# Kernel tuning notes

Measured on AMD Instinct MI355X. Metric: run time of the kernel, lower is better.

## Reference

```python
import jax, jax.numpy as jnp
import numpy as np

B, T, F, H, OUT, L = 4096, 336, 12, 50, 1, 3


def _lstm_layer(x_tbf, W_ih, W_hh, b_ih, b_hh):
    """PyTorch-semantics LSTM layer. x_tbf: [T,B,in]; returns [T,B,H]."""
    Hh = W_hh.shape[1]
    Bsz = x_tbf.shape[1]
    # precompute input projection for all timesteps: [T,B,4H]
    xz = jnp.einsum('tbf,gf->tbg', x_tbf, W_ih) + (b_ih + b_hh)

    def step(carry, xz_t):
        h, c = carry
        z = xz_t + h @ W_hh.T  # [B,4H]
        i, f, g, o = jnp.split(z, 4, axis=-1)  # PyTorch gate order i,f,g,o
        c = jax.nn.sigmoid(f) * c + jax.nn.sigmoid(i) * jnp.tanh(g)
        h = jax.nn.sigmoid(o) * jnp.tanh(c)
        return (h, c), h

    h0 = jnp.zeros((Bsz, Hh), x_tbf.dtype)
    c0 = jnp.zeros((Bsz, Hh), x_tbf.dtype)
    _, hs = jax.lax.scan(step, (h0, c0), xz)
    return hs


def setup_inputs() -> dict:
    key = jax.random.key(0)
    ks = jax.random.split(key, 16)
    s = 1.0 / np.sqrt(H)  # PyTorch LSTM init scale
    inp = {"x": jax.random.normal(ks[0], (B, T, F), dtype=jnp.float32)}
    in_sizes = [F, H, H]
    k = 1
    for l in range(L):
        inp[f"W_ih_{l}"] = jax.random.uniform(ks[k], (4 * H, in_sizes[l]), jnp.float32, -s, s); k += 1
        inp[f"W_hh_{l}"] = jax.random.uniform(ks[k], (4 * H, H), jnp.float32, -s, s); k += 1
        inp[f"b_ih_{l}"] = jax.random.uniform(ks[k], (4 * H,), jnp.float32, -s, s); k += 1
        inp[f"b_hh_{l}"] = jax.random.uniform(ks[k], (4 * H,), jnp.float32, -s, s); k += 1
    inp["W_lin"] = jax.random.uniform(ks[13], (OUT, H), jnp.float32, -s, s)
    inp["b_lin"] = jax.random.uniform(ks[14], (OUT,), jnp.float32, -s, s)
    return inp


def reference(x, W_ih_0, W_hh_0, b_ih_0, b_hh_0,
              W_ih_1, W_hh_1, b_ih_1, b_hh_1,
              W_ih_2, W_hh_2, b_ih_2, b_hh_2,
              W_lin, b_lin):
    h = jnp.transpose(x, (1, 0, 2))  # [T,B,F] time-major for scan
    params = [(W_ih_0, W_hh_0, b_ih_0, b_hh_0),
              (W_ih_1, W_hh_1, b_ih_1, b_hh_1),
              (W_ih_2, W_hh_2, b_ih_2, b_hh_2)]
    for W_ih, W_hh, bi, bh in params:
        h = _lstm_layer(h, W_ih, W_hh, bi, bh)  # [T,B,H]
    last = h[-1]  # out[:, -1, :] in batch_first layout
    return last @ W_lin.T + b_lin  # [B,OUT]
```

## Files before the change

kernel.cpp:

```cpp
#include <hip/hip_runtime.h>


#define Bsz 4096
#define Tt  336
#define BT  16
#define NTH 1024

typedef _Float16 half8 __attribute__((ext_vector_type(8)));
typedef float    floatx4 __attribute__((ext_vector_type(4)));

struct __align__(16) SMem {
  _Float16 act0[2][BT * 64];
  _Float16 act1[2][BT * 128];
  _Float16 act2[2][BT * 128];
};

__device__ __forceinline__ int offA0(int n, int L) {
  return n * 64 + ((((L >> 3) ^ n) & 7) << 3) + (L & 7);
}
__device__ __forceinline__ int offA12(int n, int L) {
  return n * 128 + ((((L >> 3) ^ n) & 15) << 3) + (L & 7);
}

__device__ __forceinline__ float lstm_cell(floatx4 z, float& c) {
  float ei = __builtin_amdgcn_exp2f(z[0]);
  float ef = __builtin_amdgcn_exp2f(z[1]);
  float eg = __builtin_amdgcn_exp2f(z[2]);
  float eo = __builtin_amdgcn_exp2f(z[3]);
  float ig = __builtin_amdgcn_rcpf(1.f + ei);
  float fg = __builtin_amdgcn_rcpf(1.f + ef);
  float rg = __builtin_amdgcn_rcpf(1.f + eg);
  float og = __builtin_amdgcn_rcpf(1.f + eo);
  float gg = 1.f - 2.f * rg;
  c = fg * c + ig * gg;
  float ec = __builtin_amdgcn_exp2f(2.885390082f * c);
  float rc = __builtin_amdgcn_rcpf(1.f + ec);
  return og * (1.f - 2.f * rc);
}

__device__ __forceinline__ half8 wfrag(const float* __restrict__ Wih,
                                       const float* __restrict__ Whh,
                                       int lenih, int bound, int R, int k0) {
  half8 r = {};
  int u = R >> 2, g = R & 3;
  float sc = (g == 2) ? 2.885390082f : -1.442695041f;
  if (u < 50) {
    int row = g * 50 + u;
#pragma unroll
    for (int j = 0; j < 8; ++j) {
      int k = k0 + j;
      float v = 0.f;
      if (k < bound)           v = Wih[row * lenih + k];
      else if (k < bound + 50) v = Whh[row * 50 + (k - bound)];
      r[j] = (_Float16)(sc * v);
    }
  }
  return r;
}

#define MFMA(a, b, acc) __builtin_amdgcn_mfma_f32_16x16x32_f16((a), (b), (acc), 0, 0, 0)

__global__ __launch_bounds__(NTH, 4)
void lstm_mfma_kernel(const float* __restrict__ x,
                      const float* __restrict__ Wih0, const float* __restrict__ Whh0,
                      const float* __restrict__ bih0, const float* __restrict__ bhh0,
                      const float* __restrict__ Wih1, const float* __restrict__ Whh1,
                      const float* __restrict__ bih1, const float* __restrict__ bhh1,
                      const float* __restrict__ Wih2, const float* __restrict__ Whh2,
                      const float* __restrict__ bih2, const float* __restrict__ bhh2,
                      const float* __restrict__ Wlin, const float* __restrict__ blin,
                      float* __restrict__ out) {
  __shared__ SMem sm;
  const int tid  = threadIdx.x;
  const int blk  = blockIdx.x;
  const int lane = tid & 63;
  const int w    = tid >> 6;
  const int n    = lane & 15;
  const int q    = lane >> 4;

  {
    int* zp = (int*)&sm;
    for (int i = tid; i < (int)(sizeof(SMem) / 4); i += NTH) zp[i] = 0;
  }

  int Lw, nc, mm3[3] = {0, 0, 0};
  switch (w) {
    case 0:  Lw = 0; nc = 3; mm3[0] = 0;  mm3[1] = 1;  mm3[2] = 2;  break;
    case 1:  Lw = 0; nc = 2; mm3[0] = 3;  mm3[1] = 4;               break;
    case 2:  Lw = 0; nc = 3; mm3[0] = 5;  mm3[1] = 6;  mm3[2] = 7;  break;
    case 3:  Lw = 0; nc = 2; mm3[0] = 8;  mm3[1] = 9;               break;
    case 4:  Lw = 1; nc = 2; mm3[0] = 0;  mm3[1] = 1;               break;
    case 5:  Lw = 1; nc = 3; mm3[0] = 2;  mm3[1] = 3;  mm3[2] = 4;  break;
    case 6:  Lw = 1; nc = 2; mm3[0] = 5;  mm3[1] = 6;               break;
    case 7:  Lw = 1; nc = 3; mm3[0] = 7;  mm3[1] = 8;  mm3[2] = 9;  break;
    case 8:  Lw = 2; nc = 3; mm3[0] = 0;  mm3[1] = 1;  mm3[2] = 2;  break;
    case 9:  Lw = 2; nc = 2; mm3[0] = 3;  mm3[1] = 4;               break;
    case 10: Lw = 2; nc = 2; mm3[0] = 5;  mm3[1] = 6;               break;
    case 11: Lw = 2; nc = 2; mm3[0] = 7;  mm3[1] = 8;               break;
    case 12: Lw = 2; nc = 2; mm3[0] = 9;  mm3[1] = 10;              break;
    case 13: Lw = 0; nc = 3; mm3[0] = 10; mm3[1] = 11; mm3[2] = 12; break;
    case 14: Lw = 1; nc = 3; mm3[0] = 10; mm3[1] = 11; mm3[2] = 12; break;
    default: Lw = 2; nc = 2; mm3[0] = 11; mm3[1] = 12;              break;
  }
  const float* Wih = (Lw == 0) ? Wih0 : ((Lw == 1) ? Wih1 : Wih2);
  const float* Whh = (Lw == 0) ? Whh0 : ((Lw == 1) ? Whh1 : Whh2);
  const float* bih = (Lw == 0) ? bih0 : ((Lw == 1) ? bih1 : bih2);
  const float* bhh = (Lw == 0) ? bhh0 : ((Lw == 1) ? bhh1 : bhh2);
  const int lenih = (Lw == 0) ? 12 : 50;
  const int nkc   = (Lw == 0) ? 2 : 4;

  half8  af[3][4];
  floatx4 bia[3];
  float  cst[3] = {0.f, 0.f, 0.f};
  int    woA[3], woB[3];
  bool   uokk[3];
#pragma unroll
  for (int i = 0; i < 3; ++i) {
    bia[i] = (floatx4){0, 0, 0, 0};
#pragma unroll
    for (int kc = 0; kc < 4; ++kc) af[i][kc] = (half8){};
    int m = mm3[i];
    int u = 4 * m + q;
    int uc = (u < 50) ? u : 49;
    uokk[i] = (i < nc) && (u < 50);
    if (Lw == 0) { woA[i] = offA0 (n, 12 + uc); woB[i] = offA12(n, uc); }
    else         { woA[i] = offA12(n, 50 + uc); woB[i] = offA12(n, uc); }
    if (i < nc) {
      int R = 16 * m + n;
#pragma unroll
      for (int kc = 0; kc < 4; ++kc)
        if (kc < nkc)
          af[i][kc] = wfrag(Wih, Whh, lenih, lenih, R, kc * 32 + q * 8);
      if (u < 50) {
#pragma unroll
        for (int g = 0; g < 4; ++g) {
          float sc = (g == 2) ? 2.885390082f : -1.442695041f;
          bia[i][g] = sc * (bih[g * 50 + u] + bhh[g * 50 + u]);
        }
      }
    }
  }

  const int ro0[2] = { offA0(n, q * 8), offA0(n, 32 + q * 8) };
  const int ro1[4] = { offA12(n, q * 8),      offA12(n, 32 + q * 8),
                       offA12(n, 64 + q * 8), offA12(n, 96 + q * 8) };

  const int sr = (tid < 192) ? tid / 12 : 0;
  const int sf = (tid < 192) ? tid - sr * 12 : 0;
  const int sxo = offA0(sr, sf);
  const float* xp = x + ((size_t)(blk * BT + sr) * Tt) * 12 + sf;
  float xnext = 0.f;

  __syncthreads();
  if (tid < 192) {
    sm.act0[0][sxo] = (_Float16)xp[0];
    xnext = xp[12];
  }
  __syncthreads();

#define TICK(p, TAU, CHK)                                                  \
  {                                                                        \
    if (Lw == 0) {                                                         \
      if (!(CHK) || (TAU) <= 335) {                                        \
        half8 b0 = *(const half8*)&sm.act0[p][ro0[0]];                     \
        half8 b1 = *(const half8*)&sm.act0[p][ro0[1]];                     \
        for (int i = 0; i < 3; ++i) if (i < nc) {                          \
          floatx4 z = bia[i];                                              \
          z = MFMA(af[i][0], b0, z);                                       \
          z = MFMA(af[i][1], b1, z);                                       \
          float h = lstm_cell(z, cst[i]);                                  \
          _Float16 hh = (_Float16)h;                                       \
          if (uokk[i]) { sm.act0[1 - (p)][woA[i]] = hh;                    \
                         sm.act1[1 - (p)][woB[i]] = hh; }                  \
        }                                                                  \
      }                                                                    \
    } else if (Lw == 1) {                                                  \
      if (!(CHK) || ((TAU) >= 1 && (TAU) <= 336)) {                        \
        half8 b0 = *(const half8*)&sm.act1[p][ro1[0]];                     \
        half8 b1 = *(const half8*)&sm.act1[p][ro1[1]];                     \
        half8 b2 = *(const half8*)&sm.act1[p][ro1[2]];                     \
        half8 b3 = *(const half8*)&sm.act1[p][ro1[3]];                     \
        for (int i = 0; i < 3; ++i) if (i < nc) {                          \
          floatx4 z = bia[i];                                              \
          z = MFMA(af[i][0], b0, z);                                       \
          z = MFMA(af[i][1], b1, z);                                       \
          z = MFMA(af[i][2], b2, z);                                       \
          z = MFMA(af[i][3], b3, z);                                       \
          float h = lstm_cell(z, cst[i]);                                  \
          _Float16 hh = (_Float16)h;                                       \
          if (uokk[i]) { sm.act1[1 - (p)][woA[i]] = hh;                    \
                         sm.act2[1 - (p)][woB[i]] = hh; }                  \
        }                                                                  \
      }                                                                    \
    } else {                                                               \
      if (!(CHK) || ((TAU) >= 2)) {                                        \
        half8 b0 = *(const half8*)&sm.act2[p][ro1[0]];                     \
        half8 b1 = *(const half8*)&sm.act2[p][ro1[1]];                     \
        half8 b2 = *(const half8*)&sm.act2[p][ro1[2]];                     \
        half8 b3 = *(const half8*)&sm.act2[p][ro1[3]];                     \
        for (int i = 0; i < 3; ++i) if (i < nc) {                          \
          floatx4 z = bia[i];                                              \
          z = MFMA(af[i][0], b0, z);                                       \
          z = MFMA(af[i][1], b1, z);                                       \
          z = MFMA(af[i][2], b2, z);                                       \
          z = MFMA(af[i][3], b3, z);                                       \
          float h = lstm_cell(z, cst[i]);                                  \
          if (uokk[i]) sm.act2[1 - (p)][woA[i]] = (_Float16)h;             \
        }                                                                  \
      }                                                                    \
    }                                                                      \
    if (tid < 192) {                                                       \
      if ((TAU) + 1 < Tt) sm.act0[1 - (p)][sxo] = (_Float16)xnext;         \
      xnext = ((TAU) + 2 < Tt) ? xp[((TAU) + 2) * 12] : 0.f;               \
    }                                                                      \
    __syncthreads();                                                       \
  }

  TICK(0, 0, 1)
  TICK(1, 1, 1)
#pragma unroll 1
  for (int t = 2; t < Tt; t += 2) {
    TICK(0, t, 0)
    TICK(1, t + 1, 0)
  }
  TICK(0, 336, 1)
  TICK(1, 337, 1)
#undef TICK

  if (tid < BT) {
    float s = blin[0];
    for (int uu = 0; uu < 50; ++uu)
      s += Wlin[uu] * (float)sm.act2[0][offA12(tid, 50 + uu)];
    out[blk * BT + tid] = s;
  }
}

extern "C" void kernel_launch(void* const* d_in, const int* in_sizes, int n_in,
                              void* d_out, int out_size, void* d_ws, size_t ws_size,
                              hipStream_t stream) {
  const float* x    = (const float*)d_in[0];
  const float* Wih0 = (const float*)d_in[1];
  const float* Whh0 = (const float*)d_in[2];
  const float* bih0 = (const float*)d_in[3];
  const float* bhh0 = (const float*)d_in[4];
  const float* Wih1 = (const float*)d_in[5];
  const float* Whh1 = (const float*)d_in[6];
  const float* bih1 = (const float*)d_in[7];
  const float* bhh1 = (const float*)d_in[8];
  const float* Wih2 = (const float*)d_in[9];
  const float* Whh2 = (const float*)d_in[10];
  const float* bih2 = (const float*)d_in[11];
  const float* bhh2 = (const float*)d_in[12];
  const float* Wlin = (const float*)d_in[13];
  const float* blin = (const float*)d_in[14];
  float* outp = (float*)d_out;

  dim3 grid(Bsz / BT);
  dim3 block(NTH);
  lstm_mfma_kernel<<<grid, block, 0, stream>>>(
      x, Wih0, Whh0, bih0, bhh0, Wih1, Whh1, bih1, bhh1,
      Wih2, Whh2, bih2, bhh2, Wlin, blin, outp);
}
```

Before: 405.3 us.

## Prefetch input-projection operands one tick ahead to deepen the layer wavefront

```diff
diff --git a/kernel.cpp b/kernel.cpp
--- a/kernel.cpp
+++ b/kernel.cpp
@@ -106,8 +106,6 @@
   const float* Whh = (Lw == 0) ? Whh0 : ((Lw == 1) ? Whh1 : Whh2);
   const float* bih = (Lw == 0) ? bih0 : ((Lw == 1) ? bih1 : bih2);
   const float* bhh = (Lw == 0) ? bhh0 : ((Lw == 1) ? bhh1 : bhh2);
-  const int lenih = (Lw == 0) ? 12 : 50;
-  const int nkc   = (Lw == 0) ? 2 : 4;
 
   half8  af[3][4];
   floatx4 bia[3];
@@ -123,14 +121,21 @@
     int u = 4 * m + q;
     int uc = (u < 50) ? u : 49;
     uokk[i] = (i < nc) && (u < 50);
-    if (Lw == 0) { woA[i] = offA0 (n, 12 + uc); woB[i] = offA12(n, uc); }
-    else         { woA[i] = offA12(n, 50 + uc); woB[i] = offA12(n, uc); }
+    if (Lw == 0) { woA[i] = offA0 (n, 12 + uc); woB[i] = offA12(n, 64 + uc); }
+    else         { woA[i] = offA12(n, uc);      woB[i] = offA12(n, 64 + uc); }
     if (i < nc) {
       int R = 16 * m + n;
-#pragma unroll
-      for (int kc = 0; kc < 4; ++kc)
-        if (kc < nkc)
-          af[i][kc] = wfrag(Wih, Whh, lenih, lenih, R, kc * 32 + q * 8);
+      if (Lw == 0) {
+#pragma unroll
+        for (int kc = 0; kc < 2; ++kc)
+          af[i][kc] = wfrag(Wih, Whh, 12, 12, R, kc * 32 + q * 8);
+      } else {
+#pragma unroll
+        for (int kc = 0; kc < 2; ++kc) {
+          af[i][kc]     = wfrag(Whh, Whh, 50, 50, R, kc * 32 + q * 8);
+          af[i][kc + 2] = wfrag(Wih, Whh, 50, 50, R, kc * 32 + q * 8);
+        }
+      }
       if (u < 50) {
 #pragma unroll
         for (int g = 0; g < 4; ++g) {
@@ -144,6 +149,8 @@
   const int ro0[2] = { offA0(n, q * 8), offA0(n, 32 + q * 8) };
   const int ro1[4] = { offA12(n, q * 8),      offA12(n, 32 + q * 8),
                        offA12(n, 64 + q * 8), offA12(n, 96 + q * 8) };
+
+  half8 bpf[2][2] = {};
 
   const int sr = (tid < 192) ? tid / 12 : 0;
   const int sf = (tid < 192) ? tid - sr * 12 : 0;
@@ -175,17 +182,22 @@
         }                                                                  \
       }                                                                    \
     } else if (Lw == 1) {                                                  \
+      half8 b0 = {}, b1 = {};                                              \
+      if (!(CHK) || ((TAU) >= 2 && (TAU) <= 337)) {                        \
+        b0 = *(const half8*)&sm.act1[p][ro1[0]];                           \
+        b1 = *(const half8*)&sm.act1[p][ro1[1]];                           \
+      }                                                                    \
       if (!(CHK) || ((TAU) >= 1 && (TAU) <= 336)) {                        \
-        half8 b0 = *(const half8*)&sm.act1[p][ro1[0]];                     \
-        half8 b1 = *(const half8*)&sm.act1[p][ro1[1]];                     \
-        half8 b2 = *(const half8*)&sm.act1[p][ro1[2]];                     \
-        half8 b3 = *(const half8*)&sm.act1[p][ro1[3]];                     \
+        bpf[1 - (p)][0] = *(const half8*)&sm.act1[p][ro1[2]];              \
+        bpf[1 - (p)][1] = *(const half8*)&sm.act1[p][ro1[3]];              \
+      }                                                                    \
+      if (!(CHK) || ((TAU) >= 2 && (TAU) <= 337)) {                        \
         for (int i = 0; i < 3; ++i) if (i < nc) {                          \
           floatx4 z = bia[i];                                              \
+          z = MFMA(af[i][2], bpf[p][0], z);                                \
+          z = MFMA(af[i][3], bpf[p][1], z);                                \
           z = MFMA(af[i][0], b0, z);                                       \
           z = MFMA(af[i][1], b1, z);                                       \
-          z = MFMA(af[i][2], b2, z);                                       \
-          z = MFMA(af[i][3], b3, z);                                       \
           float h = lstm_cell(z, cst[i]);                                  \
           _Float16 hh = (_Float16)h;                                       \
           if (uokk[i]) { sm.act1[1 - (p)][woA[i]] = hh;                    \
@@ -193,17 +205,22 @@
         }                                                                  \
       }                                                                    \
     } else {                                                               \
-      if (!(CHK) || ((TAU) >= 2)) {                                        \
-        half8 b0 = *(const half8*)&sm.act2[p][ro1[0]];                     \
-        half8 b1 = *(const half8*)&sm.act2[p][ro1[1]];                     \
-        half8 b2 = *(const half8*)&sm.act2[p][ro1[2]];                     \
-        half8 b3 = *(const half8*)&sm.act2[p][ro1[3]];                     \
+      half8 b0 = {}, b1 = {};                                              \
+      if (!(CHK) || ((TAU) >= 4 && (TAU) <= 339)) {                        \
+        b0 = *(const half8*)&sm.act2[p][ro1[0]];                           \
+        b1 = *(const half8*)&sm.act2[p][ro1[1]];                           \
+      }                                                                    \
+      if (!(CHK) || ((TAU) >= 3 && (TAU) <= 338)) {                        \
+        bpf[1 - (p)][0] = *(const half8*)&sm.act2[p][ro1[2]];              \
+        bpf[1 - (p)][1] = *(const half8*)&sm.act2[p][ro1[3]];              \
+      }                                                                    \
+      if (!(CHK) || ((TAU) >= 4 && (TAU) <= 339)) {                        \
         for (int i = 0; i < 3; ++i) if (i < nc) {                          \
           floatx4 z = bia[i];                                              \
+          z = MFMA(af[i][2], bpf[p][0], z);                                \
+          z = MFMA(af[i][3], bpf[p][1], z);                                \
           z = MFMA(af[i][0], b0, z);                                       \
           z = MFMA(af[i][1], b1, z);                                       \
-          z = MFMA(af[i][2], b2, z);                                       \
-          z = MFMA(af[i][3], b3, z);                                       \
           float h = lstm_cell(z, cst[i]);                                  \
           if (uokk[i]) sm.act2[1 - (p)][woA[i]] = (_Float16)h;             \
         }                                                                  \
@@ -218,19 +235,23 @@
 
   TICK(0, 0, 1)
   TICK(1, 1, 1)
+  TICK(0, 2, 1)
+  TICK(1, 3, 1)
 #pragma unroll 1
-  for (int t = 2; t < Tt; t += 2) {
+  for (int t = 4; t < Tt; t += 2) {
     TICK(0, t, 0)
     TICK(1, t + 1, 0)
   }
   TICK(0, 336, 1)
   TICK(1, 337, 1)
+  TICK(0, 338, 1)
+  TICK(1, 339, 1)
 #undef TICK
 
   if (tid < BT) {
     float s = blin[0];
     for (int uu = 0; uu < 50; ++uu)
-      s += Wlin[uu] * (float)sm.act2[0][offA12(tid, 50 + uu)];
+      s += Wlin[uu] * (float)sm.act2[0][offA12(tid, uu)];
     out[blk * BT + tid] = s;
   }
 }
```

Result: faster. 394.7 us, median of 3 (-2.6%).

## Split each layer's gate GEMM across waves with shared-memory partial sums

Applied to the files above, without the earlier changes.

```diff
diff --git a/kernel.cpp b/kernel.cpp
--- a/kernel.cpp
+++ b/kernel.cpp
@@ -4,22 +4,21 @@
 #define Bsz 4096
 #define Tt  336
 #define BT  16
-#define NTH 1024
+#define NTH 320
 
 typedef _Float16 half8 __attribute__((ext_vector_type(8)));
 typedef float    floatx4 __attribute__((ext_vector_type(4)));
 
 struct __align__(16) SMem {
   _Float16 act0[2][BT * 64];
-  _Float16 act1[2][BT * 128];
-  _Float16 act2[2][BT * 128];
+  _Float16 act1[2][BT * 64];
+  _Float16 act2[2][BT * 64];
+  float z1[2][13 * 256];
+  float z2[2][13 * 256];
 };
 
-__device__ __forceinline__ int offA0(int n, int L) {
+__device__ __forceinline__ int offA(int n, int L) {
   return n * 64 + ((((L >> 3) ^ n) & 7) << 3) + (L & 7);
-}
-__device__ __forceinline__ int offA12(int n, int L) {
-  return n * 128 + ((((L >> 3) ^ n) & 15) << 3) + (L & 7);
 }
 
 __device__ __forceinline__ float lstm_cell(floatx4 z, float& c) {
@@ -27,20 +26,18 @@
   float ef = __builtin_amdgcn_exp2f(z[1]);
   float eg = __builtin_amdgcn_exp2f(z[2]);
   float eo = __builtin_amdgcn_exp2f(z[3]);
-  float ig = __builtin_amdgcn_rcpf(1.f + ei);
-  float fg = __builtin_amdgcn_rcpf(1.f + ef);
-  float rg = __builtin_amdgcn_rcpf(1.f + eg);
-  float og = __builtin_amdgcn_rcpf(1.f + eo);
-  float gg = 1.f - 2.f * rg;
-  c = fg * c + ig * gg;
+  float fg  = __builtin_amdgcn_rcpf(1.f + ef);
+  float itg = (eg - 1.f) *
+              __builtin_amdgcn_rcpf((1.f + ei) * (1.f + eg));
+  c = fg * c + itg;
   float ec = __builtin_amdgcn_exp2f(2.885390082f * c);
-  float rc = __builtin_amdgcn_rcpf(1.f + ec);
-  return og * (1.f - 2.f * rc);
-}
-
-__device__ __forceinline__ half8 wfrag(const float* __restrict__ Wih,
-                                       const float* __restrict__ Whh,
-                                       int lenih, int bound, int R, int k0) {
+  return (ec - 1.f) *
+         __builtin_amdgcn_rcpf((1.f + eo) * (1.f + ec));
+}
+
+__device__ __forceinline__ half8 wfrag2(const float* __restrict__ Wa, int lena,
+                                        const float* __restrict__ Wb, int offb,
+                                        int lenb, int R, int k0) {
   half8 r = {};
   int u = R >> 2, g = R & 3;
   float sc = (g == 2) ? 2.885390082f : -1.442695041f;
@@ -50,8 +47,8 @@
     for (int j = 0; j < 8; ++j) {
       int k = k0 + j;
       float v = 0.f;
-      if (k < bound)           v = Wih[row * lenih + k];
-      else if (k < bound + 50) v = Whh[row * 50 + (k - bound)];
+      if (Wa && k < lena)                          v = Wa[row * lena + k];
+      else if (Wb && k >= offb && k < offb + lenb) v = Wb[row * lenb + (k - offb)];
       r[j] = (_Float16)(sc * v);
     }
   }
@@ -60,7 +57,7 @@
 
 #define MFMA(a, b, acc) __builtin_amdgcn_mfma_f32_16x16x32_f16((a), (b), (acc), 0, 0, 0)
 
-__global__ __launch_bounds__(NTH, 4)
+__global__ __launch_bounds__(NTH, 1)
 void lstm_mfma_kernel(const float* __restrict__ x,
                       const float* __restrict__ Wih0, const float* __restrict__ Whh0,
                       const float* __restrict__ bih0, const float* __restrict__ bhh0,
@@ -77,160 +74,161 @@
   const int w    = tid >> 6;
   const int n    = lane & 15;
   const int q    = lane >> 4;
+  const int zi   = n * 4 + q;
 
   {
     int* zp = (int*)&sm;
     for (int i = tid; i < (int)(sizeof(SMem) / 4); i += NTH) zp[i] = 0;
   }
 
-  int Lw, nc, mm3[3] = {0, 0, 0};
+  const float *WA, *WB, *bi, *bh;
+  int lena, offb, lenb;
   switch (w) {
-    case 0:  Lw = 0; nc = 3; mm3[0] = 0;  mm3[1] = 1;  mm3[2] = 2;  break;
-    case 1:  Lw = 0; nc = 2; mm3[0] = 3;  mm3[1] = 4;               break;
-    case 2:  Lw = 0; nc = 3; mm3[0] = 5;  mm3[1] = 6;  mm3[2] = 7;  break;
-    case 3:  Lw = 0; nc = 2; mm3[0] = 8;  mm3[1] = 9;               break;
-    case 4:  Lw = 1; nc = 2; mm3[0] = 0;  mm3[1] = 1;               break;
-    case 5:  Lw = 1; nc = 3; mm3[0] = 2;  mm3[1] = 3;  mm3[2] = 4;  break;
-    case 6:  Lw = 1; nc = 2; mm3[0] = 5;  mm3[1] = 6;               break;
-    case 7:  Lw = 1; nc = 3; mm3[0] = 7;  mm3[1] = 8;  mm3[2] = 9;  break;
-    case 8:  Lw = 2; nc = 3; mm3[0] = 0;  mm3[1] = 1;  mm3[2] = 2;  break;
-    case 9:  Lw = 2; nc = 2; mm3[0] = 3;  mm3[1] = 4;               break;
-    case 10: Lw = 2; nc = 2; mm3[0] = 5;  mm3[1] = 6;               break;
-    case 11: Lw = 2; nc = 2; mm3[0] = 7;  mm3[1] = 8;               break;
-    case 12: Lw = 2; nc = 2; mm3[0] = 9;  mm3[1] = 10;              break;
-    case 13: Lw = 0; nc = 3; mm3[0] = 10; mm3[1] = 11; mm3[2] = 12; break;
-    case 14: Lw = 1; nc = 3; mm3[0] = 10; mm3[1] = 11; mm3[2] = 12; break;
-    default: Lw = 2; nc = 2; mm3[0] = 11; mm3[1] = 12;              break;
-  }
-  const float* Wih = (Lw == 0) ? Wih0 : ((Lw == 1) ? Wih1 : Wih2);
-  const float* Whh = (Lw == 0) ? Whh0 : ((Lw == 1) ? Whh1 : Whh2);
-  const float* bih = (Lw == 0) ? bih0 : ((Lw == 1) ? bih1 : bih2);
-  const float* bhh = (Lw == 0) ? bhh0 : ((Lw == 1) ? bhh1 : bhh2);
-  const int lenih = (Lw == 0) ? 12 : 50;
-  const int nkc   = (Lw == 0) ? 2 : 4;
-
-  half8  af[3][4];
-  floatx4 bia[3];
-  float  cst[3] = {0.f, 0.f, 0.f};
-  int    woA[3], woB[3];
-  bool   uokk[3];
+    case 0:  WA = nullptr; lena = 0;  WB = Wih1;    offb = 12; lenb = 50;
+             bi = bih1; bh = bhh1; break;
+    case 1:  WA = Wih0;    lena = 12; WB = Whh0;    offb = 12; lenb = 50;
+             bi = bih0; bh = bhh0; break;
+    case 2:  WA = Whh1;    lena = 50; WB = nullptr; offb = 0;  lenb = 0;
+             bi = nullptr; bh = nullptr; break;
+    case 3:  WA = Whh2;    lena = 50; WB = nullptr; offb = 0;  lenb = 0;
+             bi = nullptr; bh = nullptr; break;
+    default: WA = Wih2;    lena = 50; WB = nullptr; offb = 0;  lenb = 0;
+             bi = bih2; bh = bhh2; break;
+  }
+
+  _Float16 (*pl)[BT * 64];
+  float (*zs)[13 * 256];
+  switch (w) {
+    case 0:  pl = sm.act0; zs = sm.z1; break;
+    case 1:  pl = sm.act0; zs = sm.z1; break;
+    case 2:  pl = sm.act1; zs = sm.z1; break;
+    case 3:  pl = sm.act2; zs = sm.z2; break;
+    default: pl = sm.act1; zs = sm.z2; break;
+  }
+
+  half8   af[13][2];
+  floatx4 bia[13];
+  float   cst[13];
+  int     wo[13];
+  bool    uok[13];
 #pragma unroll
-  for (int i = 0; i < 3; ++i) {
-    bia[i] = (floatx4){0, 0, 0, 0};
-#pragma unroll
-    for (int kc = 0; kc < 4; ++kc) af[i][kc] = (half8){};
-    int m = mm3[i];
+  for (int m = 0; m < 13; ++m) {
+    int R = 16 * m + n;
     int u = 4 * m + q;
     int uc = (u < 50) ? u : 49;
-    uokk[i] = (i < nc) && (u < 50);
-    if (Lw == 0) { woA[i] = offA0 (n, 12 + uc); woB[i] = offA12(n, uc); }
-    else         { woA[i] = offA12(n, 50 + uc); woB[i] = offA12(n, uc); }
-    if (i < nc) {
-      int R = 16 * m + n;
+    uok[m] = (u < 50);
+    cst[m] = 0.f;
+    bia[m] = (floatx4){0, 0, 0, 0};
+    wo[m] = (w == 1) ? offA(n, 12 + uc) : offA(n, uc);
+    af[m][0] = wfrag2(WA, lena, WB, offb, lenb, R, q * 8);
+    af[m][1] = wfrag2(WA, lena, WB, offb, lenb, R, 32 + q * 8);
+    if (bi && u < 50) {
 #pragma unroll
-      for (int kc = 0; kc < 4; ++kc)
-        if (kc < nkc)
-          af[i][kc] = wfrag(Wih, Whh, lenih, lenih, R, kc * 32 + q * 8);
-      if (u < 50) {
-#pragma unroll
-        for (int g = 0; g < 4; ++g) {
-          float sc = (g == 2) ? 2.885390082f : -1.442695041f;
-          bia[i][g] = sc * (bih[g * 50 + u] + bhh[g * 50 + u]);
-        }
+      for (int g = 0; g < 4; ++g) {
+        float sc = (g == 2) ? 2.885390082f : -1.442695041f;
+        bia[m][g] = sc * (bi[g * 50 + u] + bh[g * 50 + u]);
       }
     }
   }
 
-  const int ro0[2] = { offA0(n, q * 8), offA0(n, 32 + q * 8) };
-  const int ro1[4] = { offA12(n, q * 8),      offA12(n, 32 + q * 8),
-                       offA12(n, 64 + q * 8), offA12(n, 96 + q * 8) };
-
-  const int sr = (tid < 192) ? tid / 12 : 0;
-  const int sf = (tid < 192) ? tid - sr * 12 : 0;
-  const int sxo = offA0(sr, sf);
-  const float* xp = x + ((size_t)(blk * BT + sr) * Tt) * 12 + sf;
-  float xnext = 0.f;
+  const int ro0 = offA(n, q * 8), ro1 = offA(n, 32 + q * 8);
+
+  const int xidx = lane * 3;
+  const int r0 = xidx / 12,       f0 = xidx - r0 * 12;
+  const int r1 = (xidx + 1) / 12, f1 = (xidx + 1) - r1 * 12;
+  const int r2 = (xidx + 2) / 12, f2 = (xidx + 2) - r2 * 12;
+  const int sx0 = offA(r0, f0), sx1 = offA(r1, f1), sx2 = offA(r2, f2);
+  const float* xp0 = x + ((size_t)(blk * BT + r0) * Tt) * 12 + f0;
+  const float* xp1 = x + ((size_t)(blk * BT + r1) * Tt) * 12 + f1;
+  const float* xp2 = x + ((size_t)(blk * BT + r2) * Tt) * 12 + f2;
+  float xn0 = 0.f, xn1 = 0.f, xn2 = 0.f;
 
   __syncthreads();
-  if (tid < 192) {
-    sm.act0[0][sxo] = (_Float16)xp[0];
-    xnext = xp[12];
+  if (w == 1) {
+    sm.act0[0][sx0] = (_Float16)xp0[0];
+    sm.act0[0][sx1] = (_Float16)xp1[0];
+    sm.act0[0][sx2] = (_Float16)xp2[0];
+    xn0 = xp0[12]; xn1 = xp1[12]; xn2 = xp2[12];
   }
   __syncthreads();
 
 #define TICK(p, TAU, CHK)                                                  \
   {                                                                        \
-    if (Lw == 0) {                                                         \
+    if (w == 1) {                                                          \
       if (!(CHK) || (TAU) <= 335) {                                        \
-        half8 b0 = *(const half8*)&sm.act0[p][ro0[0]];                     \
-        half8 b1 = *(const half8*)&sm.act0[p][ro0[1]];                     \
-        for (int i = 0; i < 3; ++i) if (i < nc) {                          \
-          floatx4 z = bia[i];                                              \
-          z = MFMA(af[i][0], b0, z);                                       \
-          z = MFMA(af[i][1], b1, z);                                       \
-          float h = lstm_cell(z, cst[i]);                                  \
-          _Float16 hh = (_Float16)h;                                       \
-          if (uokk[i]) { sm.act0[1 - (p)][woA[i]] = hh;                    \
-                         sm.act1[1 - (p)][woB[i]] = hh; }                  \
+        half8 b0 = *(const half8*)&pl[p][ro0];                             \
+        half8 b1 = *(const half8*)&pl[p][ro1];                             \
+        _Float16* sw = &pl[1 - (p)][0];                                    \
+        _Pragma("unroll")                                                  \
+        for (int m = 0; m < 13; ++m) {                                     \
+          floatx4 z = bia[m];                                              \
+          z = MFMA(af[m][0], b0, z);                                       \
+          z = MFMA(af[m][1], b1, z);                                       \
+          float h = lstm_cell(z, cst[m]);                                  \
+          if (uok[m]) sw[wo[m]] = (_Float16)h;                             \
+        }                                                                  \
+        if ((TAU) + 1 < Tt) {                                              \
+          sw[sx0] = (_Float16)xn0; sw[sx1] = (_Float16)xn1;                \
+          sw[sx2] = (_Float16)xn2;                                         \
+        }                                                                  \
+        if ((TAU) + 2 < Tt) {                                              \
+          xn0 = xp0[((TAU) + 2) * 12]; xn1 = xp1[((TAU) + 2) * 12];        \
+          xn2 = xp2[((TAU) + 2) * 12];                                     \
         }                                                                  \
       }                                                                    \
-    } else if (Lw == 1) {                                                  \
-      if (!(CHK) || ((TAU) >= 1 && (TAU) <= 336)) {                        \
-        half8 b0 = *(const half8*)&sm.act1[p][ro1[0]];                     \
-        half8 b1 = *(const half8*)&sm.act1[p][ro1[1]];                     \
-        half8 b2 = *(const half8*)&sm.act1[p][ro1[2]];                     \
-        half8 b3 = *(const half8*)&sm.act1[p][ro1[3]];                     \
-        for (int i = 0; i < 3; ++i) if (i < nc) {                          \
-          floatx4 z = bia[i];                                              \
-          z = MFMA(af[i][0], b0, z);                                       \
-          z = MFMA(af[i][1], b1, z);                                       \
-          z = MFMA(af[i][2], b2, z);                                       \
-          z = MFMA(af[i][3], b3, z);                                       \
-          float h = lstm_cell(z, cst[i]);                                  \
-          _Float16 hh = (_Float16)h;                                       \
-          if (uokk[i]) { sm.act1[1 - (p)][woA[i]] = hh;                    \
-                         sm.act2[1 - (p)][woB[i]] = hh; }                  \
+    } else if (w == 0 || w == 4) {                                         \
+      if (!(CHK) || ((w == 0) ? ((TAU) >= 1 && (TAU) <= 336)               \
+                              : ((TAU) >= 3 && (TAU) <= 338))) {           \
+        half8 b0 = *(const half8*)&pl[p][ro0];                             \
+        half8 b1 = *(const half8*)&pl[p][ro1];                             \
+        floatx4* zw = (floatx4*)&zs[1 - (p)][0];                           \
+        _Pragma("unroll")                                                  \
+        for (int m = 0; m < 13; ++m) {                                     \
+          floatx4 z = bia[m];                                              \
+          z = MFMA(af[m][0], b0, z);                                       \
+          z = MFMA(af[m][1], b1, z);                                       \
+          zw[m * 64 + zi] = z;                                             \
         }                                                                  \
       }                                                                    \
     } else {                                                               \
-      if (!(CHK) || ((TAU) >= 2)) {                                        \
-        half8 b0 = *(const half8*)&sm.act2[p][ro1[0]];                     \
-        half8 b1 = *(const half8*)&sm.act2[p][ro1[1]];                     \
-        half8 b2 = *(const half8*)&sm.act2[p][ro1[2]];                     \
-        half8 b3 = *(const half8*)&sm.act2[p][ro1[3]];                     \
-        for (int i = 0; i < 3; ++i) if (i < nc) {                          \
-          floatx4 z = bia[i];                                              \
-          z = MFMA(af[i][0], b0, z);                                       \
-          z = MFMA(af[i][1], b1, z);                                       \
-          z = MFMA(af[i][2], b2, z);                                       \
-          z = MFMA(af[i][3], b3, z);                                       \
-          float h = lstm_cell(z, cst[i]);                                  \
-          if (uokk[i]) sm.act2[1 - (p)][woA[i]] = (_Float16)h;             \
+      if (!(CHK) || ((w == 2) ? ((TAU) >= 2 && (TAU) <= 337)               \
+                              : ((TAU) >= 4 && (TAU) <= 339))) {           \
+        half8 b0 = *(const half8*)&pl[p][ro0];                             \
+        half8 b1 = *(const half8*)&pl[p][ro1];                             \
+        const floatx4* zr = (const floatx4*)&zs[p][0];                     \
+        _Float16* sw = &pl[1 - (p)][0];                                    \
+        _Pragma("unroll")                                                  \
+        for (int m = 0; m < 13; ++m) {                                     \
+          floatx4 z = zr[m * 64 + zi];                                     \
+          z = MFMA(af[m][0], b0, z);                                       \
+          z = MFMA(af[m][1], b1, z);                                       \
+          float h = lstm_cell(z, cst[m]);                                  \
+          if (uok[m]) sw[wo[m]] = (_Float16)h;                             \
         }                                                                  \
       }                                                                    \
     }                                                                      \
-    if (tid < 192) {                                                       \
-      if ((TAU) + 1 < Tt) sm.act0[1 - (p)][sxo] = (_Float16)xnext;         \
-      xnext = ((TAU) + 2 < Tt) ? xp[((TAU) + 2) * 12] : 0.f;               \
-    }                                                                      \
     __syncthreads();                                                       \
   }
 
   TICK(0, 0, 1)
   TICK(1, 1, 1)
+  TICK(0, 2, 1)
+  TICK(1, 3, 1)
 #pragma unroll 1
-  for (int t = 2; t < Tt; t += 2) {
+  for (int t = 4; t < Tt; t += 2) {
     TICK(0, t, 0)
     TICK(1, t + 1, 0)
   }
   TICK(0, 336, 1)
   TICK(1, 337, 1)
+  TICK(0, 338, 1)
+  TICK(1, 339, 1)
 #undef TICK
 
   if (tid < BT) {
     float s = blin[0];
     for (int uu = 0; uu < 50; ++uu)
-      s += Wlin[uu] * (float)sm.act2[0][offA12(tid, 50 + uu)];
+      s += Wlin[uu] * (float)sm.act2[0][offA(tid, uu)];
     out[blk * BT + tid] = s;
   }
 }
```

New measurement: 679.6 us. 67.7% more time.
